# Kernel optimization log

Measured on AMD Instinct MI355X. Metric: run time of the kernel, lower is better.

The kernel has to match this reference:

```python
import jax, jax.numpy as jnp
import numpy as np

EPS = 1e-10
LOSS_COEF = 0.01

def cv_squared(v):
    # torch .var() is unbiased (ddof=1)
    return jnp.var(v, ddof=1) / (jnp.mean(v) ** 2 + EPS)

def setup_inputs() -> dict:
    B, Q, D, H, O, E = 4096, 256, 512, 1024, 512, 16
    key = jax.random.key(0)
    ks = jax.random.split(key, 8)
    return {
        "query": jax.random.normal(ks[0], (B, Q), jnp.float32),
        "x": jax.random.normal(ks[1], (B, D), jnp.float32),
        "w_gate": jax.random.normal(ks[2], (D, E), jnp.float32) * 0.02,
        "task_gate": jax.random.normal(ks[3], (Q, E), jnp.float32) * 0.02,
        "W1": jax.random.normal(ks[4], (E, D, H), jnp.float32) * 0.02,
        "b1": jnp.zeros((E, H), jnp.float32),
        "W2": jax.random.normal(ks[5], (E, H, O), jnp.float32) * 0.02,
        "b2": jnp.zeros((E, O), jnp.float32),
        "k": 4,
    }

def reference(query, x, w_gate, task_gate, W1, b1, W2, b2, k):
    B = x.shape[0]
    E = w_gate.shape[1]
    # --- top-k gating (eval mode: clean logits, no noise) ---
    logits = x @ w_gate + query @ task_gate                      # [B, E]
    m = min(k + 1, E)
    top_vals, top_idx = jax.lax.top_k(logits, m)                 # [B, m]
    topk_gates = jax.nn.softmax(top_vals[:, :k], axis=1)         # [B, k]
    rows = jnp.arange(B)[:, None]
    gates = jnp.zeros_like(logits).at[rows, top_idx[:, :k]].set(topk_gates)  # [B, E]
    importance = gates.sum(0)                                    # [E]
    load = (gates > 0).sum(0).astype(jnp.float32)                # [E]
    loss = LOSS_COEF * (cv_squared(importance) + cv_squared(load))
    # --- dispatch / expert MLP / combine ---
    # gate==0 contributions vanish, so weighting by gates is exactly
    # equivalent to the sparse gather -> expert -> index_add combine.
    y = jnp.zeros((B, W2.shape[2]), jnp.float32)
    for e in range(E):  # fixed small loop over experts
        h = jax.nn.relu(x @ W1[e] + b1[e])                       # [B, H]
        out = h @ W2[e] + b2[e]                                  # [B, O]
        y = y + gates[:, e:e + 1] * out
    return y, loss
```

## Files before the change

kernel.cpp:

```cpp
#include <hip/hip_runtime.h>

typedef short bf16x8_t __attribute__((ext_vector_type(8)));
typedef float f32x4_t __attribute__((ext_vector_type(4)));

#define B_DIM 4096
#define Q_DIM 256
#define D_DIM 512
#define H_DIM 1024
#define O_DIM 512
#define E_NUM 16
#define K_TOP 4

#define BM 128
#define BN 128
#define BK 32

__device__ __forceinline__ short f2bf(float f) {
  unsigned int u = __float_as_uint(f);
  u += 0x7FFFu + ((u >> 16) & 1u);
  return (short)(u >> 16);
}

__device__ __forceinline__ void g2l16(const void* g, void* l) {
  __builtin_amdgcn_global_load_lds(
      (const __attribute__((address_space(1))) void*)(unsigned long long)(size_t)g,
      (__attribute__((address_space(3))) void*)(unsigned)(size_t)l, 16, 0, 0);
}

__global__ __launch_bounds__(256) void prep_kernel(const float* __restrict__ x,
                                                   const float* __restrict__ wg,
                                                   const float* __restrict__ tg,
                                                   short* __restrict__ x_bf,
                                                   float* __restrict__ wpack) {
  const int blk = blockIdx.x, t = threadIdx.x;
  if (blk < 1024) {
    int base = blk * 2048 + t * 8;
    float4 f0 = *(const float4*)(x + base);
    float4 f1 = *(const float4*)(x + base + 4);
    bf16x8_t v;
    v[0] = f2bf(f0.x); v[1] = f2bf(f0.y); v[2] = f2bf(f0.z); v[3] = f2bf(f0.w);
    v[4] = f2bf(f1.x); v[5] = f2bf(f1.y); v[6] = f2bf(f1.z); v[7] = f2bf(f1.w);
    *(bf16x8_t*)(x_bf + base) = v;
  } else {
    int lin = (blk - 1024) * 256 + t;
    if (lin < E_NUM * 768) {
      int e = lin / 768, r = lin % 768;
      wpack[lin] = (r < D_DIM) ? wg[r * E_NUM + e] : tg[(r - D_DIM) * E_NUM + e];
    }
  }
}

__global__ __launch_bounds__(256) void transpose_cvt(const float* __restrict__ src,
                                                     short* __restrict__ dst, int R, int C) {
  __shared__ float tile[64][65];
  const int e = blockIdx.z;
  const int r0 = blockIdx.y * 64, c0 = blockIdx.x * 64;
  const int t = threadIdx.x;
  const float* s = src + (size_t)e * R * C;
  short* d = dst + (size_t)e * R * C;
#pragma unroll
  for (int i = 0; i < 16; i++) {
    int lin = i * 256 + t;
    int rr = lin >> 6, cc = lin & 63;
    tile[rr][cc] = s[(size_t)(r0 + rr) * C + (c0 + cc)];
  }
  __syncthreads();
#pragma unroll
  for (int i = 0; i < 16; i++) {
    int lin = i * 256 + t;
    int cr = lin >> 6, rc = lin & 63;
    d[(size_t)(c0 + cr) * R + (r0 + rc)] = f2bf(tile[rc][cr]);
  }
}

__global__ __launch_bounds__(256) void gating_kernel(
    const float* __restrict__ x, const float* __restrict__ query,
    const float* __restrict__ wpack,
    int4* __restrict__ topk_e4, float4* __restrict__ topk_g4) {
  __shared__ __align__(16) float4 s_w[E_NUM * 192];
  const int t = threadIdx.x, wv = t >> 6, lane = t & 63;
  const float4* wp4 = (const float4*)wpack;
#pragma unroll
  for (int i = 0; i < 12; i++) s_w[i * 256 + t] = wp4[i * 256 + t];
  __syncthreads();

  const int row = blockIdx.x * 4 + wv;
  const float4* xr = (const float4*)(x + (size_t)row * D_DIM);
  const float4* qr = (const float4*)(query + (size_t)row * Q_DIM);
  const float4 xv0 = xr[lane], xv1 = xr[64 + lane], qv = qr[lane];

  float p[E_NUM];
#pragma unroll
  for (int e = 0; e < E_NUM; e++) {
    float4 w0 = s_w[e * 192 + lane];
    float4 w1 = s_w[e * 192 + 64 + lane];
    float4 wq = s_w[e * 192 + 128 + lane];
    p[e] = xv0.x * w0.x + xv0.y * w0.y + xv0.z * w0.z + xv0.w * w0.w +
           xv1.x * w1.x + xv1.y * w1.y + xv1.z * w1.z + xv1.w * w1.w +
           qv.x * wq.x + qv.y * wq.y + qv.z * wq.z + qv.w * wq.w;
  }
#pragma unroll
  for (int e = 0; e < E_NUM; e++) {
    p[e] += __shfl_xor(p[e], 16, 64);
    p[e] += __shfl_xor(p[e], 32, 64);
  }
#pragma unroll
  for (int s = 8; s >= 1; s >>= 1) {
    const bool take = (lane & s) != 0;
#pragma unroll
    for (int j = 0; j < s; j++) {
      float keep = take ? p[j + s] : p[j];
      float send = take ? p[j] : p[j + s];
      p[j] = keep + __shfl_xor(send, s, 64);
    }
  }
  const float logit = p[0];
  float v[E_NUM];
#pragma unroll
  for (int i = 0; i < E_NUM; i++) v[i] = __shfl(logit, i, 64);

  if (lane == 0) {
    int idx[K_TOP];
    float val[K_TOP];
    unsigned used = 0;
    for (int k = 0; k < K_TOP; k++) {
      float best = -3.4e38f;
      int bi = 0;
      for (int i = 0; i < E_NUM; i++)
        if (!(used & (1u << i)) && v[i] > best) { best = v[i]; bi = i; }
      used |= 1u << bi;
      idx[k] = bi;
      val[k] = best;
    }
    float mx = val[0];
    float ex[K_TOP], Z = 0.f;
    for (int k = 0; k < K_TOP; k++) { ex[k] = __expf(val[k] - mx); Z += ex[k]; }
    topk_e4[row] = make_int4(idx[0], idx[1], idx[2], idx[3]);
    topk_g4[row] = make_float4(ex[0] / Z, ex[1] / Z, ex[2] / Z, ex[3] / Z);
  }
}

__global__ __launch_bounds__(256) void csr_kernel(
    const int4* __restrict__ topk_e4, const float4* __restrict__ topk_g4,
    int* __restrict__ count, float* __restrict__ imp_g,
    int* __restrict__ rowlist, int* __restrict__ slotid, float* __restrict__ egate) {
  const int e = blockIdx.x, t = threadIdx.x;
  __shared__ int s_cnt[256];
  __shared__ float s_gs[64];
  int c = 0;
  float gs = 0.f;
#pragma unroll 4
  for (int i = 0; i < 16; i++) {
    int row = t * 16 + i;
    int4 v = topk_e4[row];
    float4 g = topk_g4[row];
    if (v.x == e) { c++; gs += g.x; }
    if (v.y == e) { c++; gs += g.y; }
    if (v.z == e) { c++; gs += g.z; }
    if (v.w == e) { c++; gs += g.w; }
  }
  s_cnt[t] = c;
  float gw = gs;
  for (int off = 32; off >= 1; off >>= 1) gw += __shfl_down(gw, off, 64);
  if ((t & 63) == 0) s_gs[t >> 6] = gw;
  __syncthreads();
  for (int off = 1; off < 256; off <<= 1) {
    int vv = (t >= off) ? s_cnt[t - off] : 0;
    __syncthreads();
    s_cnt[t] += vv;
    __syncthreads();
  }
  int pos = s_cnt[t] - c;
#pragma unroll 4
  for (int i = 0; i < 16; i++) {
    int row = t * 16 + i;
    int4 v = topk_e4[row];
    float4 g = topk_g4[row];
    int ve[4] = {v.x, v.y, v.z, v.w};
    float vg[4] = {g.x, g.y, g.z, g.w};
#pragma unroll
    for (int k = 0; k < K_TOP; k++) {
      if (ve[k] == e) {
        rowlist[e * B_DIM + pos] = row;
        slotid[e * B_DIM + pos] = row * K_TOP + k;
        egate[e * B_DIM + pos] = vg[k];
        pos++;
      }
    }
  }
  if (t == 0) {
    count[e] = s_cnt[255];
    imp_g[e] = s_gs[0] + s_gs[1] + s_gs[2] + s_gs[3];
  }
}

__global__ __launch_bounds__(64) void loss_offsets_kernel(
    const int* __restrict__ count, const float* __restrict__ imp_g,
    int* __restrict__ offs, float* __restrict__ out_loss) {
  if (threadIdx.x == 0) {
    float mi = 0.f, ml = 0.f;
    for (int i = 0; i < E_NUM; i++) { mi += imp_g[i]; ml += (float)count[i]; }
    mi /= (float)E_NUM;
    ml /= (float)E_NUM;
    float vi = 0.f, vl = 0.f;
    for (int i = 0; i < E_NUM; i++) {
      float di = imp_g[i] - mi;
      vi += di * di;
      float dl = (float)count[i] - ml;
      vl += dl * dl;
    }
    vi /= (float)(E_NUM - 1);
    vl /= (float)(E_NUM - 1);
    out_loss[0] = 0.01f * (vi / (mi * mi + 1e-10f) + vl / (ml * ml + 1e-10f));
    int run = 0;
    for (int i = 0; i < E_NUM; i++) { offs[i] = run; run += count[i]; }
  }
}

__global__ __launch_bounds__(256) void gemm1_kernel(
    const short* __restrict__ x_bf, const short* __restrict__ w1t,
    const float* __restrict__ b1, const int* __restrict__ count,
    const int* __restrict__ offs, const int* __restrict__ rowlist,
    short* __restrict__ h_buf) {
  const int e = blockIdx.z, mt = blockIdx.y, nt = blockIdx.x;
  const int n_e = count[e];
  if (mt * BM >= n_e) return;
  __shared__ __align__(16) short As[BM * BK];
  __shared__ __align__(16) short Bs[BN * BK];
  const int t = threadIdx.x, lane = t & 63, wv = t >> 6;
  const int wm = wv >> 1, wn = wv & 1;
  const int srow = wv * 16 + (lane >> 2);
  const int kb = (lane & 3) * 8;
  int gr0 = mt * BM + srow;       gr0 = gr0 < n_e ? gr0 : n_e - 1;
  int gr1 = mt * BM + 64 + srow;  gr1 = gr1 < n_e ? gr1 : n_e - 1;
  const short* pa0 = x_bf + (size_t)rowlist[e * B_DIM + gr0] * D_DIM + kb;
  const short* pa1 = x_bf + (size_t)rowlist[e * B_DIM + gr1] * D_DIM + kb;
  const short* w1te = w1t + ((size_t)e * H_DIM + nt * BN) * D_DIM;
  const short* pb0 = w1te + (size_t)srow * D_DIM + kb;
  const short* pb1 = w1te + (size_t)(64 + srow) * D_DIM + kb;
  short* lA0 = As + wv * 16 * BK;
  short* lA1 = As + (64 + wv * 16) * BK;
  short* lB0 = Bs + wv * 16 * BK;
  short* lB1 = Bs + (64 + wv * 16) * BK;

  f32x4_t acc[4][4] = {};
  const int frow = lane & 15, kg = lane >> 4;

  for (int k0 = 0; k0 < D_DIM; k0 += BK) {
    g2l16(pa0 + k0, lA0);
    g2l16(pa1 + k0, lA1);
    g2l16(pb0 + k0, lB0);
    g2l16(pb1 + k0, lB1);
    __syncthreads();
    bf16x8_t af[4], bfr[4];
#pragma unroll
    for (int mi = 0; mi < 4; mi++)
      af[mi] = *(const bf16x8_t*)&As[(wm * 64 + mi * 16 + frow) * BK + kg * 8];
#pragma unroll
    for (int ni = 0; ni < 4; ni++)
      bfr[ni] = *(const bf16x8_t*)&Bs[(wn * 64 + ni * 16 + frow) * BK + kg * 8];
#pragma unroll
    for (int mi = 0; mi < 4; mi++)
#pragma unroll
      for (int ni = 0; ni < 4; ni++)
        acc[mi][ni] = __builtin_amdgcn_mfma_f32_16x16x32_bf16(af[mi], bfr[ni], acc[mi][ni], 0, 0, 0);
    __syncthreads();
  }
  const int obase = offs[e];
#pragma unroll
  for (int mi = 0; mi < 4; mi++) {
#pragma unroll
    for (int r = 0; r < 4; r++) {
      int row = wm * 64 + mi * 16 + kg * 4 + r;
      int m_local = mt * BM + row;
      if (m_local >= n_e) continue;
      size_t hrow = (size_t)(obase + m_local) * H_DIM;
#pragma unroll
      for (int ni = 0; ni < 4; ni++) {
        int col = nt * BN + wn * 64 + ni * 16 + frow;
        float vv = acc[mi][ni][r] + b1[e * H_DIM + col];
        h_buf[hrow + col] = f2bf(vv > 0.f ? vv : 0.f);
      }
    }
  }
}

__global__ __launch_bounds__(256) void gemm2_kernel(
    const short* __restrict__ h_buf, const short* __restrict__ w2t,
    const float* __restrict__ b2, const int* __restrict__ count,
    const int* __restrict__ offs, const int* __restrict__ slotid,
    const float* __restrict__ egate, float* __restrict__ out_buf) {
  const int e = blockIdx.z, mt = blockIdx.y, nt = blockIdx.x;
  const int n_e = count[e];
  if (mt * BM >= n_e) return;
  __shared__ __align__(16) short As[BM * BK];
  __shared__ __align__(16) short Bs[BN * BK];
  const int t = threadIdx.x, lane = t & 63, wv = t >> 6;
  const int wm = wv >> 1, wn = wv & 1;
  const int srow = wv * 16 + (lane >> 2);
  const int kb = (lane & 3) * 8;
  const int obase = offs[e];
  int gr0 = mt * BM + srow;       gr0 = gr0 < n_e ? gr0 : n_e - 1;
  int gr1 = mt * BM + 64 + srow;  gr1 = gr1 < n_e ? gr1 : n_e - 1;
  const short* pa0 = h_buf + (size_t)(obase + gr0) * H_DIM + kb;
  const short* pa1 = h_buf + (size_t)(obase + gr1) * H_DIM + kb;
  const short* w2te = w2t + ((size_t)e * O_DIM + nt * BN) * H_DIM;
  const short* pb0 = w2te + (size_t)srow * H_DIM + kb;
  const short* pb1 = w2te + (size_t)(64 + srow) * H_DIM + kb;
  short* lA0 = As + wv * 16 * BK;
  short* lA1 = As + (64 + wv * 16) * BK;
  short* lB0 = Bs + wv * 16 * BK;
  short* lB1 = Bs + (64 + wv * 16) * BK;

  f32x4_t acc[4][4] = {};
  const int frow = lane & 15, kg = lane >> 4;

  for (int k0 = 0; k0 < H_DIM; k0 += BK) {
    g2l16(pa0 + k0, lA0);
    g2l16(pa1 + k0, lA1);
    g2l16(pb0 + k0, lB0);
    g2l16(pb1 + k0, lB1);
    __syncthreads();
    bf16x8_t af[4], bfr[4];
#pragma unroll
    for (int mi = 0; mi < 4; mi++)
      af[mi] = *(const bf16x8_t*)&As[(wm * 64 + mi * 16 + frow) * BK + kg * 8];
#pragma unroll
    for (int ni = 0; ni < 4; ni++)
      bfr[ni] = *(const bf16x8_t*)&Bs[(wn * 64 + ni * 16 + frow) * BK + kg * 8];
#pragma unroll
    for (int mi = 0; mi < 4; mi++)
#pragma unroll
      for (int ni = 0; ni < 4; ni++)
        acc[mi][ni] = __builtin_amdgcn_mfma_f32_16x16x32_bf16(af[mi], bfr[ni], acc[mi][ni], 0, 0, 0);
    __syncthreads();
  }
#pragma unroll
  for (int mi = 0; mi < 4; mi++) {
#pragma unroll
    for (int r = 0; r < 4; r++) {
      int row = wm * 64 + mi * 16 + kg * 4 + r;
      int m_local = mt * BM + row;
      if (m_local >= n_e) continue;
      float g = egate[e * B_DIM + m_local];
      size_t orow = (size_t)slotid[e * B_DIM + m_local] * O_DIM;
#pragma unroll
      for (int ni = 0; ni < 4; ni++) {
        int col = nt * BN + wn * 64 + ni * 16 + frow;
        out_buf[orow + col] = (acc[mi][ni][r] + b2[e * O_DIM + col]) * g;
      }
    }
  }
}

__global__ __launch_bounds__(256) void combine_kernel(const float* __restrict__ out_buf,
                                                      float* __restrict__ y) {
  int idx = blockIdx.x * 256 + threadIdx.x;
  int b = idx >> 7;
  int o = (idx & 127) << 2;
  const float* base = out_buf + (size_t)b * K_TOP * O_DIM + o;
  float4 a0 = *(const float4*)(base);
  float4 a1 = *(const float4*)(base + O_DIM);
  float4 a2 = *(const float4*)(base + 2 * O_DIM);
  float4 a3 = *(const float4*)(base + 3 * O_DIM);
  float4 r;
  r.x = a0.x + a1.x + a2.x + a3.x;
  r.y = a0.y + a1.y + a2.y + a3.y;
  r.z = a0.z + a1.z + a2.z + a3.z;
  r.w = a0.w + a1.w + a2.w + a3.w;
  *(float4*)(y + (size_t)b * O_DIM + o) = r;
}

extern "C" void kernel_launch(void* const* d_in, const int* in_sizes, int n_in,
                              void* d_out, int out_size, void* d_ws, size_t ws_size,
                              hipStream_t stream) {
  (void)in_sizes; (void)n_in; (void)out_size; (void)ws_size;
  const float* query = (const float*)d_in[0];
  const float* x = (const float*)d_in[1];
  const float* wg = (const float*)d_in[2];
  const float* tg = (const float*)d_in[3];
  const float* W1 = (const float*)d_in[4];
  const float* b1 = (const float*)d_in[5];
  const float* W2 = (const float*)d_in[6];
  const float* b2 = (const float*)d_in[7];
  float* y = (float*)d_out;

  char* ws = (char*)d_ws;
  int* count = (int*)(ws + 0);
  float* imp = (float*)(ws + 64);
  int* offs = (int*)(ws + 128);
  int* rowlist = (int*)(ws + 256);
  int* slotid = (int*)(ws + 262400);
  float* egate = (float*)(ws + 524544);
  int4* topk_e4 = (int4*)(ws + 786688);
  float4* topk_g4 = (float4*)(ws + 852224);
  float* wpack = (float*)(ws + 917760);
  short* h_buf = (short*)(ws + 1048576);
  short* w2t = (short*)(ws + 34603008);
  short* x_bf = (short*)(ws + 51380224);
  short* w1t = (short*)(ws + 55574528);
  float* out_buf = (float*)(ws + 51380224);

  prep_kernel<<<dim3(1072), 256, 0, stream>>>(x, wg, tg, x_bf, wpack);
  transpose_cvt<<<dim3(H_DIM / 64, D_DIM / 64, E_NUM), 256, 0, stream>>>(W1, w1t, D_DIM, H_DIM);
  transpose_cvt<<<dim3(O_DIM / 64, H_DIM / 64, E_NUM), 256, 0, stream>>>(W2, w2t, H_DIM, O_DIM);
  gating_kernel<<<dim3(B_DIM / 4), 256, 0, stream>>>(x, query, wpack, topk_e4, topk_g4);
  csr_kernel<<<dim3(E_NUM), 256, 0, stream>>>(topk_e4, topk_g4, count, imp,
                                              rowlist, slotid, egate);
  loss_offsets_kernel<<<1, 64, 0, stream>>>(count, imp, offs, y + (size_t)B_DIM * O_DIM);
  gemm1_kernel<<<dim3(H_DIM / BN, B_DIM / BM, E_NUM), 256, 0, stream>>>(
      x_bf, w1t, b1, count, offs, rowlist, h_buf);
  gemm2_kernel<<<dim3(O_DIM / BN, B_DIM / BM, E_NUM), 256, 0, stream>>>(
      h_buf, w2t, b2, count, offs, slotid, egate, out_buf);
  combine_kernel<<<dim3(B_DIM * O_DIM / 4 / 256), 256, 0, stream>>>(out_buf, y);
}
```

Baseline: 251.5 us.

## Fuse weight prep kernels, fold x bf16 cast into gating, XCD-aware GEMM grids

Combines the W1/W2 transpose-convert and gate weight packing into one launch, and moves the x-to-bf16 conversion into the gating kernel so x is read once. The transpose now writes 16-byte vectorized bf16 stores instead of scalar shorts. The two expert GEMMs switch to a flat 1D grid remapped so that blocks sharing an expert/weight tile land on the same XCD, which is meant to improve L2 reuse of weights. This cuts launch count and redundant traffic, at the cost of more complex index math and strided LDS reads during the transpose.

Result: faster. 235.8 us (-6.2%).

```diff
diff --git a/kernel.cpp b/kernel.cpp
--- a/kernel.cpp
+++ b/kernel.cpp
@@ -1,6 +1,7 @@
 #include <hip/hip_runtime.h>
 
 typedef short bf16x8_t __attribute__((ext_vector_type(8)));
+typedef short bf16x4_t __attribute__((ext_vector_type(4)));
 typedef float f32x4_t __attribute__((ext_vector_type(4)));
 
 #define B_DIM 4096
@@ -27,37 +28,9 @@
       (__attribute__((address_space(3))) void*)(unsigned)(size_t)l, 16, 0, 0);
 }
 
-__global__ __launch_bounds__(256) void prep_kernel(const float* __restrict__ x,
-                                                   const float* __restrict__ wg,
-                                                   const float* __restrict__ tg,
-                                                   short* __restrict__ x_bf,
-                                                   float* __restrict__ wpack) {
-  const int blk = blockIdx.x, t = threadIdx.x;
-  if (blk < 1024) {
-    int base = blk * 2048 + t * 8;
-    float4 f0 = *(const float4*)(x + base);
-    float4 f1 = *(const float4*)(x + base + 4);
-    bf16x8_t v;
-    v[0] = f2bf(f0.x); v[1] = f2bf(f0.y); v[2] = f2bf(f0.z); v[3] = f2bf(f0.w);
-    v[4] = f2bf(f1.x); v[5] = f2bf(f1.y); v[6] = f2bf(f1.z); v[7] = f2bf(f1.w);
-    *(bf16x8_t*)(x_bf + base) = v;
-  } else {
-    int lin = (blk - 1024) * 256 + t;
-    if (lin < E_NUM * 768) {
-      int e = lin / 768, r = lin % 768;
-      wpack[lin] = (r < D_DIM) ? wg[r * E_NUM + e] : tg[(r - D_DIM) * E_NUM + e];
-    }
-  }
-}
-
-__global__ __launch_bounds__(256) void transpose_cvt(const float* __restrict__ src,
-                                                     short* __restrict__ dst, int R, int C) {
-  __shared__ float tile[64][65];
-  const int e = blockIdx.z;
-  const int r0 = blockIdx.y * 64, c0 = blockIdx.x * 64;
-  const int t = threadIdx.x;
-  const float* s = src + (size_t)e * R * C;
-  short* d = dst + (size_t)e * R * C;
+__device__ __forceinline__ void tr_tile(float (*tile)[65], const float* __restrict__ s,
+                                        short* __restrict__ d, int R, int C, int r0, int c0,
+                                        int t) {
 #pragma unroll
   for (int i = 0; i < 16; i++) {
     int lin = i * 256 + t;
@@ -66,17 +39,46 @@
   }
   __syncthreads();
 #pragma unroll
-  for (int i = 0; i < 16; i++) {
-    int lin = i * 256 + t;
-    int cr = lin >> 6, rc = lin & 63;
-    d[(size_t)(c0 + cr) * R + (r0 + rc)] = f2bf(tile[rc][cr]);
+  for (int i = 0; i < 2; i++) {
+    int task = i * 256 + t;
+    int cr = task >> 3, g = task & 7;
+    bf16x8_t v;
+#pragma unroll
+    for (int j = 0; j < 8; j++) v[j] = f2bf(tile[g * 8 + j][cr]);
+    *(bf16x8_t*)(d + (size_t)(c0 + cr) * R + r0 + g * 8) = v;
+  }
+}
+
+__global__ __launch_bounds__(256) void weights_prep(
+    const float* __restrict__ W1, const float* __restrict__ W2,
+    const float* __restrict__ wg, const float* __restrict__ tg,
+    short* __restrict__ w1t, short* __restrict__ w2t, float* __restrict__ wpack) {
+  __shared__ float tile[64][65];
+  const int blk = blockIdx.x, t = threadIdx.x;
+  if (blk < 2048) {
+    int e = blk >> 7, rem = blk & 127;
+    int r0 = (rem >> 4) * 64, c0 = (rem & 15) * 64;
+    tr_tile(tile, W1 + (size_t)e * D_DIM * H_DIM, w1t + (size_t)e * D_DIM * H_DIM,
+            D_DIM, H_DIM, r0, c0, t);
+  } else if (blk < 4096) {
+    int b2 = blk - 2048;
+    int e = b2 >> 7, rem = b2 & 127;
+    int r0 = (rem >> 3) * 64, c0 = (rem & 7) * 64;
+    tr_tile(tile, W2 + (size_t)e * H_DIM * O_DIM, w2t + (size_t)e * H_DIM * O_DIM,
+            H_DIM, O_DIM, r0, c0, t);
+  } else {
+    int lin = (blk - 4096) * 256 + t;
+    if (lin < E_NUM * 768) {
+      int e = lin / 768, r = lin % 768;
+      wpack[lin] = (r < D_DIM) ? wg[r * E_NUM + e] : tg[(r - D_DIM) * E_NUM + e];
+    }
   }
 }
 
 __global__ __launch_bounds__(256) void gating_kernel(
     const float* __restrict__ x, const float* __restrict__ query,
     const float* __restrict__ wpack,
-    int4* __restrict__ topk_e4, float4* __restrict__ topk_g4) {
+    int4* __restrict__ topk_e4, float4* __restrict__ topk_g4, short* __restrict__ x_bf) {
   __shared__ __align__(16) float4 s_w[E_NUM * 192];
   const int t = threadIdx.x, wv = t >> 6, lane = t & 63;
   const float4* wp4 = (const float4*)wpack;
@@ -88,6 +90,15 @@
   const float4* xr = (const float4*)(x + (size_t)row * D_DIM);
   const float4* qr = (const float4*)(query + (size_t)row * Q_DIM);
   const float4 xv0 = xr[lane], xv1 = xr[64 + lane], qv = qr[lane];
+
+  {
+    bf16x4_t v0, v1;
+    v0[0] = f2bf(xv0.x); v0[1] = f2bf(xv0.y); v0[2] = f2bf(xv0.z); v0[3] = f2bf(xv0.w);
+    v1[0] = f2bf(xv1.x); v1[1] = f2bf(xv1.y); v1[2] = f2bf(xv1.z); v1[3] = f2bf(xv1.w);
+    short* xb = x_bf + (size_t)row * D_DIM;
+    *(bf16x4_t*)(xb + lane * 4) = v0;
+    *(bf16x4_t*)(xb + 256 + lane * 4) = v1;
+  }
 
   float p[E_NUM];
 #pragma unroll
@@ -222,7 +233,11 @@
     const float* __restrict__ b1, const int* __restrict__ count,
     const int* __restrict__ offs, const int* __restrict__ rowlist,
     short* __restrict__ h_buf) {
-  const int e = blockIdx.z, mt = blockIdx.y, nt = blockIdx.x;
+  const int flat = blockIdx.x;
+  const int xcd = flat & 7, j = flat >> 3;
+  const int mt = j & 31, gidx = j >> 5;
+  const int group = xcd * 16 + gidx;
+  const int e = group >> 3, nt = group & 7;
   const int n_e = count[e];
   if (mt * BM >= n_e) return;
   __shared__ __align__(16) short As[BM * BK];
@@ -290,7 +305,11 @@
     const float* __restrict__ b2, const int* __restrict__ count,
     const int* __restrict__ offs, const int* __restrict__ slotid,
     const float* __restrict__ egate, float* __restrict__ out_buf) {
-  const int e = blockIdx.z, mt = blockIdx.y, nt = blockIdx.x;
+  const int flat = blockIdx.x;
+  const int xcd = flat & 7, j = flat >> 3;
+  const int nt = j & 3, gidx = j >> 2;
+  const int group = xcd * 64 + gidx;
+  const int e = group >> 5, mt = group & 31;
   const int n_e = count[e];
   if (mt * BM >= n_e) return;
   __shared__ __align__(16) short As[BM * BK];
@@ -401,16 +420,13 @@
   short* w1t = (short*)(ws + 55574528);
   float* out_buf = (float*)(ws + 51380224);
 
-  prep_kernel<<<dim3(1072), 256, 0, stream>>>(x, wg, tg, x_bf, wpack);
-  transpose_cvt<<<dim3(H_DIM / 64, D_DIM / 64, E_NUM), 256, 0, stream>>>(W1, w1t, D_DIM, H_DIM);
-  transpose_cvt<<<dim3(O_DIM / 64, H_DIM / 64, E_NUM), 256, 0, stream>>>(W2, w2t, H_DIM, O_DIM);
-  gating_kernel<<<dim3(B_DIM / 4), 256, 0, stream>>>(x, query, wpack, topk_e4, topk_g4);
+  weights_prep<<<dim3(4144), 256, 0, stream>>>(W1, W2, wg, tg, w1t, w2t, wpack);
+  gating_kernel<<<dim3(B_DIM / 4), 256, 0, stream>>>(x, query, wpack, topk_e4, topk_g4, x_bf);
   csr_kernel<<<dim3(E_NUM), 256, 0, stream>>>(topk_e4, topk_g4, count, imp,
                                               rowlist, slotid, egate);
   loss_offsets_kernel<<<1, 64, 0, stream>>>(count, imp, offs, y + (size_t)B_DIM * O_DIM);
-  gemm1_kernel<<<dim3(H_DIM / BN, B_DIM / BM, E_NUM), 256, 0, stream>>>(
-      x_bf, w1t, b1, count, offs, rowlist, h_buf);
-  gemm2_kernel<<<dim3(O_DIM / BN, B_DIM / BM, E_NUM), 256, 0, stream>>>(
-      h_buf, w2t, b2, count, offs, slotid, egate, out_buf);
+  gemm1_kernel<<<dim3(4096), 256, 0, stream>>>(x_bf, w1t, b1, count, offs, rowlist, h_buf);
+  gemm2_kernel<<<dim3(2048), 256, 0, stream>>>(h_buf, w2t, b2, count, offs, slotid, egate,
+                                               out_buf);
   combine_kernel<<<dim3(B_DIM * O_DIM / 4 / 256), 256, 0, stream>>>(out_buf, y);
 }
```
